# Optimization experiments

Hardware: AMD Instinct MI355X
Metric: run time of the kernel (lower is better)

Reference implementation:

```python
import jax, jax.numpy as jnp
import numpy as np

N_NODES = 100000
N_EDGES = 6400000
IN_CH = 128
NEG_SLOPE = 0.2


def setup_inputs() -> dict:
    key = jax.random.key(0)
    k1, k2, k3, k4, k5 = jax.random.split(key, 5)
    x = jax.random.normal(k1, (N_NODES, IN_CH), dtype=jnp.float32)
    edge_index = jax.random.randint(k2, (2, N_EDGES), 0, N_NODES, dtype=jnp.int64)
    # GATConv params (heads=1, out_channels=1): glorot-style scale
    W = jax.random.normal(k3, (IN_CH, 1), dtype=jnp.float32) / np.sqrt(IN_CH)
    att_src = jax.random.normal(k4, (1,), dtype=jnp.float32)
    att_dst = jax.random.normal(k5, (1,), dtype=jnp.float32)
    bias = jnp.zeros((1,), dtype=jnp.float32)
    return {"x": x, "edge_index": edge_index, "W": W,
            "att_src": att_src, "att_dst": att_dst, "bias": bias}


def reference(x, edge_index, W, att_src, att_dst, bias):
    N = x.shape[0]
    h = (x @ W)[:, 0]                      # [N] projected features (out_channels=1)
    # add self-loops (PyG default add_self_loops=True)
    loop = jnp.arange(N, dtype=edge_index.dtype)
    src = jnp.concatenate([edge_index[0], loop])   # [E+N]
    dst = jnp.concatenate([edge_index[1], loop])
    a_s = h * att_src[0]                   # per-node src attention term
    a_d = h * att_dst[0]                   # per-node dst attention term
    logits = jax.nn.leaky_relu(a_s[src] + a_d[dst], NEG_SLOPE)  # [E+N]
    # segment softmax over incoming edges of each destination node
    seg_max = jax.ops.segment_max(logits, dst, num_segments=N)
    e = jnp.exp(logits - seg_max[dst])
    denom = jax.ops.segment_sum(e, dst, num_segments=N)
    alpha = e / (denom[dst] + 1e-16)
    # scatter-aggregate weighted source features
    out = jax.ops.segment_sum(alpha * h[src], dst, num_segments=N)  # [N]
    return out[:, None] + bias             # [N, 1]
```

## Files before the change

kernel.cpp:

```cpp
#include <hip/hip_runtime.h>

#define IN_CH 128
#define NEG_SLOPE 0.2f
#define BINSZ 8000
#define NBINS 13
#define NW 8192
#define MAX_SG 39
#define MAX_BPB 40
#define PLACE_BLOCKS (NW / 4)
#define HMAX_BLOCKS 120
#define F_NUM 2097152.0f
#define F_DEN 16777216.0f
#define INV_F_NUM 4.76837158203125e-7f
#define INV_F_DEN 5.9604644775390625e-8f

typedef int   vi4 __attribute__((ext_vector_type(4)));
typedef float vf4 __attribute__((ext_vector_type(4)));

__device__ __forceinline__ float lrelu(float v) { return v > 0.f ? v : NEG_SLOPE * v; }
__device__ __forceinline__ unsigned enc_max(float f) {
    unsigned u = __float_as_uint(f);
    return (u & 0x80000000u) ? ~u : (u | 0x80000000u);
}
__device__ __forceinline__ float dec_max(unsigned e) {
    return (e & 0x80000000u) ? __uint_as_float(e ^ 0x80000000u) : __uint_as_float(~e);
}
__device__ __forceinline__ unsigned bf16_rne(float f) {
    unsigned u = __float_as_uint(f);
    return (u + 0x7FFFu + ((u >> 16) & 1u)) >> 16;
}

__device__ __forceinline__ void do_proj(const float* __restrict__ x, const float* __restrict__ W,
                                        const float* __restrict__ att_dst,
                                        float* __restrict__ h, float* __restrict__ ad_h,
                                        int n, int wid, int nwaves) {
    int lane = threadIdx.x & 63;
    int half = lane >> 5;
    int hl   = lane & 31;

    vf4 w4 = reinterpret_cast<const vf4*>(W)[hl];
    const float ad = att_dst[0];

    int npair = n >> 1;
    for (int p0 = wid * 4; p0 < npair; p0 += nwaves * 4) {
        float s[4];
        #pragma unroll
        for (int k = 0; k < 4; ++k) {
            int p = p0 + k;
            s[k] = 0.f;
            if (p < npair) {
                int row = 2 * p + half;
                vf4 v = __builtin_nontemporal_load(
                    reinterpret_cast<const vf4*>(x + (size_t)row * IN_CH) + hl);
                s[k] = v.x * w4.x + v.y * w4.y + v.z * w4.z + v.w * w4.w;
            }
        }
        #pragma unroll
        for (int k = 0; k < 4; ++k) {
            #pragma unroll
            for (int off = 16; off > 0; off >>= 1) s[k] += __shfl_xor(s[k], off);
        }
        #pragma unroll
        for (int k = 0; k < 4; ++k) {
            int p = p0 + k;
            if (p < npair && hl == 0) {
                int row = 2 * p + half;
                h[row] = s[k];
                ad_h[row] = s[k] * ad;
            }
        }
    }
    if ((n & 1) && wid == 0) {
        int row = n - 1;
        vf4 v = reinterpret_cast<const vf4*>(x + (size_t)row * IN_CH)[hl];
        float s = v.x * w4.x + v.y * w4.y + v.z * w4.z + v.w * w4.w;
        #pragma unroll
        for (int off = 16; off > 0; off >>= 1) s += __shfl_xor(s, off);
        if (lane == 0) { h[row] = s; ad_h[row] = s * ad; }
    }
}

__global__ __launch_bounds__(256)
void proj_kernel(const float* __restrict__ x, const float* __restrict__ W,
                 const float* __restrict__ att_dst,
                 float* __restrict__ h, float* __restrict__ ad_h, int n) {
    int wid    = (blockIdx.x * blockDim.x + threadIdx.x) >> 6;
    int nwaves = (gridDim.x * blockDim.x) >> 6;
    do_proj(x, W, att_dst, h, ad_h, n, wid, nwaves);
}

__global__ __launch_bounds__(256)
void count_proj_kernel(const int* __restrict__ dst_idx, int* __restrict__ wc, int E,
                       const float* __restrict__ x, const float* __restrict__ W,
                       const float* __restrict__ att_dst,
                       float* __restrict__ h, float* __restrict__ ad_h, int n) {
    __shared__ int cnt[4][NBINS];
    int b = blockIdx.x;
    int role = b % 3;
    if (role == 2) {
        int qid = b / 3;
        int wid = qid * 4 + (threadIdx.x >> 6);
        do_proj(x, W, att_dst, h, ad_h, n, wid, 4096);
        return;
    }
    int pid  = (b / 3) * 2 + role;
    int lane = threadIdx.x & 63, wv = threadIdx.x >> 6;
    int g = pid * 4 + wv;
    if (lane < NBINS) cnt[wv][lane] = 0;

    long long E4 = E >> 2;
    long long e0 = 4 * (E4 * g / NW);
    long long e1 = (g == NW - 1) ? (long long)E : 4 * (E4 * (g + 1) / NW);
    for (long long i0 = e0; i0 < e1; i0 += 256) {
        long long i = i0 + 4 * lane;
        if (i < e1) {
            vi4 d4 = __builtin_nontemporal_load(reinterpret_cast<const vi4*>(dst_idx + i));
            atomicAdd(&cnt[wv][d4.x / BINSZ], 1);
            atomicAdd(&cnt[wv][d4.y / BINSZ], 1);
            atomicAdd(&cnt[wv][d4.z / BINSZ], 1);
            atomicAdd(&cnt[wv][d4.w / BINSZ], 1);
        }
    }
    if (lane < NBINS) wc[lane * NW + g] = cnt[wv][lane];
}

__global__ __launch_bounds__(256)
void scanA_kernel(const int* __restrict__ wc, int* __restrict__ bsum) {
    __shared__ int wt[4];
    int t = threadIdx.x, lane = t & 63, wv = t >> 6;
    vi4 c = *reinterpret_cast<const vi4*>(wc + blockIdx.x * 1024 + 4 * t);
    int s = c.x + c.y + c.z + c.w;
    #pragma unroll
    for (int off = 32; off > 0; off >>= 1) s += __shfl_xor(s, off);
    if (lane == 0) wt[wv] = s;
    __syncthreads();
    if (t == 0) bsum[blockIdx.x] = wt[0] + wt[1] + wt[2] + wt[3];
}

__global__ __launch_bounds__(128)
void scanB_kernel(const int* __restrict__ bsum, int* __restrict__ bbase,
                  int* __restrict__ rbase, int* __restrict__ hist,
                  unsigned* __restrict__ maxenc, int nchunk) {
    __shared__ int sb[129];
    __shared__ int wt[2];
    int t = threadIdx.x, lane = t & 63, wv = t >> 6;
    if (t < 2) maxenc[t] = 0u;
    int v = (t < nchunk) ? bsum[t] : 0;
    int inc = v;
    #pragma unroll
    for (int d2 = 1; d2 < 64; d2 <<= 1) { int u = __shfl_up(inc, d2); if (lane >= d2) inc += u; }
    if (lane == 63) wt[wv] = inc;
    __syncthreads();
    int excl = ((wv == 1) ? wt[0] : 0) + inc - v;
    sb[t] = excl;
    if (t == 127) sb[128] = excl + v;
    __syncthreads();
    if (t < nchunk) bbase[t] = sb[t];
    if (t < NBINS) {
        int rb = sb[t * (NW / 1024)];
        rbase[t] = rb;
        int nb = (t == NBINS - 1) ? sb[128] : sb[(t + 1) * (NW / 1024)];
        hist[t] = nb - rb;
    }
}

__global__ __launch_bounds__(256)
void scanC_kernel(const int* __restrict__ wc, const int* __restrict__ bbase,
                  int* __restrict__ wbase) {
    __shared__ int wt[4];
    int t = threadIdx.x, lane = t & 63, wv = t >> 6;
    int base = blockIdx.x * 1024 + 4 * t;
    vi4 c = *reinterpret_cast<const vi4*>(wc + base);
    int s0 = c.x, s1 = s0 + c.y, s2 = s1 + c.z, s3 = s2 + c.w;
    int tot = s3;
    int inc = tot;
    #pragma unroll
    for (int d2 = 1; d2 < 64; d2 <<= 1) { int u = __shfl_up(inc, d2); if (lane >= d2) inc += u; }
    if (lane == 63) wt[wv] = inc;
    __syncthreads();
    int wb = 0;
    for (int k = 0; k < wv; ++k) wb += wt[k];
    int excl = bbase[blockIdx.x] + wb + inc - tot;
    vi4 o; o.x = excl; o.y = excl + s0; o.z = excl + s1; o.w = excl + s2;
    *reinterpret_cast<vi4*>(wbase + base) = o;
}

__global__ __launch_bounds__(256)
void place_hmax_kernel(const int* __restrict__ src_idx, const int* __restrict__ dst_idx,
                       const float* __restrict__ h, const int* __restrict__ wbase,
                       unsigned* __restrict__ rec, int E,
                       const float* __restrict__ att_src, const float* __restrict__ att_dst,
                       unsigned* __restrict__ maxenc, int n) {
    int b = blockIdx.x;
    if (b >= PLACE_BLOCKS) {
        int bid = b - PLACE_BLOCKS;
        const float as = att_src[0];
        const float ad = att_dst[0];
        float m1 = -1e30f, m2 = -1e30f;
        for (int i = bid * 256 + threadIdx.x; i < n; i += HMAX_BLOCKS * 256) {
            float v = h[i];
            m1 = fmaxf(m1, v * as);
            m2 = fmaxf(m2, v * ad);
        }
        #pragma unroll
        for (int off = 32; off > 0; off >>= 1) {
            m1 = fmaxf(m1, __shfl_xor(m1, off));
            m2 = fmaxf(m2, __shfl_xor(m2, off));
        }
        __shared__ float bm[2][4];
        int wv = threadIdx.x >> 6;
        if ((threadIdx.x & 63) == 0) { bm[0][wv] = m1; bm[1][wv] = m2; }
        __syncthreads();
        if (threadIdx.x == 0) {
            float a = fmaxf(fmaxf(bm[0][0], bm[0][1]), fmaxf(bm[0][2], bm[0][3]));
            float bmax = fmaxf(fmaxf(bm[1][0], bm[1][1]), fmaxf(bm[1][2], bm[1][3]));
            atomicMax(maxenc,     enc_max(a));
            atomicMax(maxenc + 1, enc_max(bmax));
        }
        return;
    }

    __shared__ int ccur[4][NBINS];
    int lane = threadIdx.x & 63, wv = threadIdx.x >> 6;
    int g = b * 4 + wv;
    if (lane < NBINS) ccur[wv][lane] = wbase[lane * NW + g];
    __syncthreads();

    long long E4 = E >> 2;
    long long e0 = 4 * (E4 * g / NW);
    long long e1 = (g == NW - 1) ? (long long)E : 4 * (E4 * (g + 1) / NW);

    long long i = e0 + 4 * (long long)lane;
    bool have = (i < e1);
    vi4 d4 = {0,0,0,0}, s4 = {0,0,0,0};
    if (have) {
        d4 = __builtin_nontemporal_load(reinterpret_cast<const vi4*>(dst_idx + i));
        s4 = __builtin_nontemporal_load(reinterpret_cast<const vi4*>(src_idx + i));
    }
    while (have) {
        long long nx = i + 256;
        bool nhave = (nx < e1);
        vi4 d4n = {0,0,0,0}, s4n = {0,0,0,0};
        if (nhave) {
            d4n = __builtin_nontemporal_load(reinterpret_cast<const vi4*>(dst_idx + nx));
            s4n = __builtin_nontemporal_load(reinterpret_cast<const vi4*>(src_idx + nx));
        }
        float h0 = h[s4.x], h1 = h[s4.y], h2 = h[s4.z], h3 = h[s4.w];
        int b0 = d4.x / BINSZ, b1 = d4.y / BINSZ, b2 = d4.z / BINSZ, b3 = d4.w / BINSZ;
        int p0 = atomicAdd(&ccur[wv][b0], 1);
        int p1 = atomicAdd(&ccur[wv][b1], 1);
        int p2 = atomicAdd(&ccur[wv][b2], 1);
        int p3 = atomicAdd(&ccur[wv][b3], 1);
        rec[p0] = ((unsigned)(d4.x - b0 * BINSZ) << 16) | bf16_rne(h0);
        rec[p1] = ((unsigned)(d4.y - b1 * BINSZ) << 16) | bf16_rne(h1);
        rec[p2] = ((unsigned)(d4.z - b2 * BINSZ) << 16) | bf16_rne(h2);
        rec[p3] = ((unsigned)(d4.w - b3 * BINSZ) << 16) | bf16_rne(h3);
        i = nx; d4 = d4n; s4 = s4n; have = nhave;
    }
}

__global__ __launch_bounds__(1024)
void gather_kernel(const unsigned* __restrict__ rec,
                   const float* __restrict__ ad_h,
                   const float* __restrict__ att_src, const unsigned* __restrict__ maxenc,
                   const int* __restrict__ rbase, const int* __restrict__ hist,
                   unsigned long long* __restrict__ part, int SG) {
    __shared__ __align__(16) unsigned long long s_acc[BINSZ];

    int bin   = blockIdx.x / SG;
    int slice = blockIdx.x - bin * SG;
    long long r0 = rbase[bin];
    int cnt   = hist[bin];
    long long g0 = r0 + (long long)cnt * slice / SG;
    long long g1 = r0 + (long long)cnt * (slice + 1) / SG;

    {
        vi4 z = {0, 0, 0, 0};
        for (int k = threadIdx.x; k < BINSZ / 2; k += 1024)
            *reinterpret_cast<vi4*>(&s_acc[2 * k]) = z;
    }
    __syncthreads();

    const float as = att_src[0];
    const float L  = lrelu(dec_max(maxenc[0]) + dec_max(maxenc[1]));
    const float* adw = ad_h + bin * BINSZ;

    auto process1 = [&](unsigned q) {
        int ri = q >> 16;
        float h0 = __uint_as_float(q << 16);
        float e0 = __expf(lrelu(fmaf(h0, as, adw[ri])) - L);
        unsigned long long p0 = ((unsigned long long)(long long)__float2int_rn(e0 * h0 * F_NUM) << 32)
                              + __float2uint_rn(e0 * F_DEN);
        atomicAdd(&s_acc[ri], p0);
    };

    long long a0 = (g0 + 3) & ~3LL;
    long long a1 = g1 & ~3LL;
    long long headEnd, tail0;
    if (a0 <= a1) { headEnd = a0; tail0 = a1; }
    else          { headEnd = g1; tail0 = g1; a0 = 0; a1 = 0; }

    for (long long i = g0 + threadIdx.x; i < headEnd; i += 1024) process1(rec[i]);

    long long i = a0 + 4 * (long long)threadIdx.x;
    vi4 q = {0,0,0,0};
    bool have = (i < a1);
    if (have) q = __builtin_nontemporal_load(reinterpret_cast<const vi4*>(rec + i));
    while (have) {
        long long nx = i + 4096;
        bool nhave = (nx < a1);
        vi4 nq = {0,0,0,0};
        if (nhave) nq = __builtin_nontemporal_load(reinterpret_cast<const vi4*>(rec + nx));
        unsigned u0=(unsigned)q.x, u1=(unsigned)q.y, u2=(unsigned)q.z, u3=(unsigned)q.w;
        int r0i=u0>>16, r1i=u1>>16, r2i=u2>>16, r3i=u3>>16;
        float h0=__uint_as_float(u0<<16), h1=__uint_as_float(u1<<16);
        float h2=__uint_as_float(u2<<16), h3=__uint_as_float(u3<<16);
        float e0 = __expf(lrelu(fmaf(h0, as, adw[r0i])) - L);
        float e1 = __expf(lrelu(fmaf(h1, as, adw[r1i])) - L);
        float e2 = __expf(lrelu(fmaf(h2, as, adw[r2i])) - L);
        float e3 = __expf(lrelu(fmaf(h3, as, adw[r3i])) - L);
        unsigned long long p0 = ((unsigned long long)(long long)__float2int_rn(e0 * h0 * F_NUM) << 32) + __float2uint_rn(e0 * F_DEN);
        unsigned long long p1 = ((unsigned long long)(long long)__float2int_rn(e1 * h1 * F_NUM) << 32) + __float2uint_rn(e1 * F_DEN);
        unsigned long long p2 = ((unsigned long long)(long long)__float2int_rn(e2 * h2 * F_NUM) << 32) + __float2uint_rn(e2 * F_DEN);
        unsigned long long p3 = ((unsigned long long)(long long)__float2int_rn(e3 * h3 * F_NUM) << 32) + __float2uint_rn(e3 * F_DEN);
        atomicAdd(&s_acc[r0i], p0);
        atomicAdd(&s_acc[r1i], p1);
        atomicAdd(&s_acc[r2i], p2);
        atomicAdd(&s_acc[r3i], p3);
        i = nx; q = nq; have = nhave;
    }

    for (long long i2 = tail0 + threadIdx.x; i2 < g1; i2 += 1024) process1(rec[i2]);
    __syncthreads();

    unsigned long long* outp = part + (size_t)blockIdx.x * BINSZ;
    for (int k = threadIdx.x; k < BINSZ / 2; k += 1024) {
        vi4 v = *reinterpret_cast<const vi4*>(&s_acc[2 * k]);
        __builtin_nontemporal_store(v, reinterpret_cast<vi4*>(outp + 2 * k));
    }
}

__global__ void reduce_final(const unsigned long long* __restrict__ part,
                             const float* __restrict__ h,
                             const float* __restrict__ att_src, const float* __restrict__ att_dst,
                             const float* __restrict__ bias, const unsigned* __restrict__ maxenc,
                             float* __restrict__ out, int n, int SG) {
    int i = blockIdx.x * blockDim.x + threadIdx.x;
    if (i >= n) return;
    int bin = i / BINSZ;
    int off = i - bin * BINSZ;
    float num = 0.f, den = 0.f;
    const unsigned long long* p = part + (size_t)(bin * SG) * BINSZ;
    for (int s = 0; s < SG; ++s) {
        unsigned long long v = __builtin_nontemporal_load(p + off);
        num += (float)(int)(v >> 32);
        den += (float)(unsigned)(v & 0xffffffffULL);
        p += BINSZ;
    }
    num *= INV_F_NUM;
    den *= INV_F_DEN;
    const float L = lrelu(dec_max(maxenc[0]) + dec_max(maxenc[1]));
    float hv = h[i];
    float e  = __expf(lrelu(hv * (att_src[0] + att_dst[0])) - L);
    out[i] = (num + e * hv) / (den + e + 1e-30f) + bias[0];
}

__global__ __launch_bounds__(1024)
void binpass_kernel(const int* __restrict__ src_idx, const int* __restrict__ dst_idx,
                    const float* __restrict__ h,
                    const float* __restrict__ att_src, const float* __restrict__ att_dst,
                    float* __restrict__ part, int E, int n, int BPB) {
    __shared__ float s_num[BINSZ];
    __shared__ float s_den[BINSZ];

    int bin   = blockIdx.x / BPB;
    int slice = blockIdx.x - bin * BPB;
    int base  = bin * BINSZ;
    int blen  = min(BINSZ, n - base);

    for (int k = threadIdx.x; k < BINSZ; k += 1024) { s_num[k] = 0.f; s_den[k] = 0.f; }
    __syncthreads();

    const float as = att_src[0];
    const float ad = att_dst[0];

    long long e0 = (long long)E * slice / BPB;
    long long e1 = (long long)E * (slice + 1) / BPB;
    for (long long i = e0 + threadIdx.x; i < e1; i += 1024) {
        int d = dst_idx[i];
        unsigned r = (unsigned)(d - base);
        if (r < (unsigned)blen) {
            int s = src_idx[i];
            float hs = h[s];
            float v  = fmaf(hs, as, h[d] * ad);
            float e  = __expf(lrelu(v));
            atomicAdd(&s_num[r], e * hs);
            atomicAdd(&s_den[r], e);
        }
    }
    __syncthreads();

    float* outp = part + (size_t)blockIdx.x * (2 * BINSZ);
    for (int k = threadIdx.x; k < BINSZ; k += 1024) {
        outp[k]         = s_num[k];
        outp[BINSZ + k] = s_den[k];
    }
}

__global__ void fb_reduce_final(const float* __restrict__ part, const float* __restrict__ h,
                                const float* __restrict__ att_src, const float* __restrict__ att_dst,
                                const float* __restrict__ bias, float* __restrict__ out,
                                int n, int BPB) {
    int i = blockIdx.x * blockDim.x + threadIdx.x;
    if (i >= n) return;
    int bin = i / BINSZ;
    int off = i - bin * BINSZ;
    float num = 0.f, den = 0.f;
    const float* p = part + (size_t)(bin * BPB) * (2 * BINSZ);
    for (int s = 0; s < BPB; ++s) {
        num += p[off];
        den += p[BINSZ + off];
        p += 2 * BINSZ;
    }
    float hv = h[i];
    float e  = __expf(lrelu(hv * (att_src[0] + att_dst[0])));
    out[i] = (num + e * hv) / (den + e + 1e-16f) + bias[0];
}

__global__ void edge_kernel(const int* __restrict__ src_idx, const int* __restrict__ dst_idx,
                            const float* __restrict__ h,
                            const float* __restrict__ att_src, const float* __restrict__ att_dst,
                            float* __restrict__ nd, int E) {
    const float as = att_src[0];
    const float ad = att_dst[0];
    int i      = blockIdx.x * blockDim.x + threadIdx.x;
    int stride = gridDim.x * blockDim.x;
    for (; i < E; i += stride) {
        int s = src_idx[i];
        int d = dst_idx[i];
        float hs = h[s];
        float e  = __expf(lrelu(fmaf(hs, as, h[d] * ad)));
        unsafeAtomicAdd(&nd[2 * d],     e * hs);
        unsafeAtomicAdd(&nd[2 * d + 1], e);
    }
}

__global__ void final_kernel(const float* __restrict__ h, const float* __restrict__ nd,
                             const float* __restrict__ att_src, const float* __restrict__ att_dst,
                             const float* __restrict__ bias, float* __restrict__ out, int n) {
    int i = blockIdx.x * blockDim.x + threadIdx.x;
    if (i >= n) return;
    float hv = h[i];
    float e  = __expf(lrelu(hv * (att_src[0] + att_dst[0])));
    out[i] = (nd[2 * i] + e * hv) / (nd[2 * i + 1] + e + 1e-16f) + bias[0];
}

extern "C" void kernel_launch(void* const* d_in, const int* in_sizes, int n_in,
                              void* d_out, int out_size, void* d_ws, size_t ws_size,
                              hipStream_t stream) {
    const float* x       = (const float*)d_in[0];
    const int*   ei      = (const int*)d_in[1];
    const float* W       = (const float*)d_in[2];
    const float* att_src = (const float*)d_in[3];
    const float* att_dst = (const float*)d_in[4];
    const float* bias    = (const float*)d_in[5];
    float*       out     = (float*)d_out;

    const int n = out_size;
    const int E = in_sizes[1] / 2;

    const int NELEM  = NBINS * NW;
    const int NCHUNK = NELEM / 1024;

    size_t off = 0;
    auto alloc = [&](size_t bytes) { size_t p = off; off = (off + bytes + 255) & ~(size_t)255; return p; };
    size_t o_h    = alloc((size_t)n * sizeof(float));
    size_t o_adh  = alloc((size_t)n * sizeof(float));
    size_t o_wc   = alloc((size_t)NELEM * sizeof(int));
    size_t o_wb   = alloc((size_t)NELEM * sizeof(int));
    size_t o_bs   = alloc((size_t)NCHUNK * sizeof(int));
    size_t o_bb   = alloc((size_t)NCHUNK * sizeof(int));
    size_t o_meta = alloc(64 * sizeof(int));
    size_t o_rec  = alloc((size_t)E * sizeof(unsigned));
    size_t fixed  = off;

    float*    h      = (float*)((char*)d_ws + o_h);
    float*    ad_h   = (float*)((char*)d_ws + o_adh);
    int*      rbase  = (int*)((char*)d_ws + o_meta);
    int*      hist   = rbase + 16;
    unsigned* maxenc = (unsigned*)(rbase + 32);
    const size_t per = (size_t)BINSZ * sizeof(unsigned long long);

    int SG = 0;
    if (ws_size > fixed) SG = (int)((ws_size - fixed) / ((size_t)NBINS * per));
    if (SG > MAX_SG) SG = MAX_SG;

    bool ok_shape = (n <= NBINS * BINSZ) && ((E & 3) == 0) && (E >= 4 * NW) && ((n & 1) == 0);

    if (SG >= 8 && ok_shape) {
        int*                wc   = (int*)((char*)d_ws + o_wc);
        int*                wb   = (int*)((char*)d_ws + o_wb);
        int*                bsum = (int*)((char*)d_ws + o_bs);
        int*                bbase= (int*)((char*)d_ws + o_bb);
        unsigned*           rec  = (unsigned*)((char*)d_ws + o_rec);
        unsigned long long* part = (unsigned long long*)((char*)d_ws + fixed);

        count_proj_kernel<<<3072, 256, 0, stream>>>(ei + E, wc, E,
                                                    x, W, att_dst, h, ad_h, n);
        scanA_kernel<<<NCHUNK, 256, 0, stream>>>(wc, bsum);
        scanB_kernel<<<1, 128, 0, stream>>>(bsum, bbase, rbase, hist, maxenc, NCHUNK);
        scanC_kernel<<<NCHUNK, 256, 0, stream>>>(wc, bbase, wb);
        place_hmax_kernel<<<PLACE_BLOCKS + HMAX_BLOCKS, 256, 0, stream>>>(
            ei, ei + E, h, wb, rec, E, att_src, att_dst, maxenc, n);
        gather_kernel<<<NBINS * SG, 1024, 0, stream>>>(rec, ad_h, att_src, maxenc,
                                                       rbase, hist, part, SG);
        reduce_final<<<(n + 255) / 256, 256, 0, stream>>>(part, h, att_src, att_dst,
                                                          bias, maxenc, out, n, SG);
    } else {
        proj_kernel<<<1024, 256, 0, stream>>>(x, W, att_dst, h, ad_h, n);
        size_t hb = (((size_t)n * 2 * sizeof(float)) + 255) & ~(size_t)255;
        int BPB = 0;
        if (ws_size > hb) BPB = (int)((ws_size - hb) / ((size_t)NBINS * per));
        if (BPB > MAX_BPB) BPB = MAX_BPB;

        if (BPB >= 6 && n <= NBINS * BINSZ) {
            float* part = (float*)((char*)d_ws + hb);
            binpass_kernel<<<NBINS * BPB, 1024, 0, stream>>>(
                ei, ei + E, h, att_src, att_dst, part, E, n, BPB);
            fb_reduce_final<<<(n + 255) / 256, 256, 0, stream>>>(
                part, h, att_src, att_dst, bias, out, n, BPB);
        } else {
            float* nd = (float*)((char*)d_ws + hb);
            hipMemsetAsync(nd, 0, (size_t)n * 2 * sizeof(float), stream);
            edge_kernel<<<2048, 256, 0, stream>>>(ei, ei + E, h, att_src, att_dst, nd, E);
            final_kernel<<<(n + 255) / 256, 256, 0, stream>>>(h, nd, att_src, att_dst,
                                                              bias, out, n);
        }
    }
}
```

Baseline: 116.5 us.

## Split placement and gather into halves to overlap second placement with first gather

Edge placement is split into two launches covering the first and second half of the wave groups. The gather for records placed by the first half runs in the same launch as the second half of placement, and a final kernel gathers the second half. The aim is to overlap scatter-placement memory traffic with the shared-memory atomic gather, at the cost of one more launch, doubled partial buffers, a longer reduce loop, and 1024-thread place blocks. Each half uses half as many gather slices per bin.

```diff
diff --git a/kernel.cpp b/kernel.cpp
--- a/kernel.cpp
+++ b/kernel.cpp
@@ -5,10 +5,10 @@
 #define BINSZ 8000
 #define NBINS 13
 #define NW 8192
-#define MAX_SG 39
+#define MAX_SGH 39
 #define MAX_BPB 40
-#define PLACE_BLOCKS (NW / 4)
-#define HMAX_BLOCKS 120
+#define PB1024 256
+#define HMAXB 30
 #define F_NUM 2097152.0f
 #define F_DEN 16777216.0f
 #define INV_F_NUM 4.76837158203125e-7f
@@ -185,50 +185,18 @@
     *reinterpret_cast<vi4*>(wbase + base) = o;
 }
 
-__global__ __launch_bounds__(256)
-void place_hmax_kernel(const int* __restrict__ src_idx, const int* __restrict__ dst_idx,
-                       const float* __restrict__ h, const int* __restrict__ wbase,
-                       unsigned* __restrict__ rec, int E,
-                       const float* __restrict__ att_src, const float* __restrict__ att_dst,
-                       unsigned* __restrict__ maxenc, int n) {
-    int b = blockIdx.x;
-    if (b >= PLACE_BLOCKS) {
-        int bid = b - PLACE_BLOCKS;
-        const float as = att_src[0];
-        const float ad = att_dst[0];
-        float m1 = -1e30f, m2 = -1e30f;
-        for (int i = bid * 256 + threadIdx.x; i < n; i += HMAX_BLOCKS * 256) {
-            float v = h[i];
-            m1 = fmaxf(m1, v * as);
-            m2 = fmaxf(m2, v * ad);
-        }
-        #pragma unroll
-        for (int off = 32; off > 0; off >>= 1) {
-            m1 = fmaxf(m1, __shfl_xor(m1, off));
-            m2 = fmaxf(m2, __shfl_xor(m2, off));
-        }
-        __shared__ float bm[2][4];
-        int wv = threadIdx.x >> 6;
-        if ((threadIdx.x & 63) == 0) { bm[0][wv] = m1; bm[1][wv] = m2; }
-        __syncthreads();
-        if (threadIdx.x == 0) {
-            float a = fmaxf(fmaxf(bm[0][0], bm[0][1]), fmaxf(bm[0][2], bm[0][3]));
-            float bmax = fmaxf(fmaxf(bm[1][0], bm[1][1]), fmaxf(bm[1][2], bm[1][3]));
-            atomicMax(maxenc,     enc_max(a));
-            atomicMax(maxenc + 1, enc_max(bmax));
-        }
-        return;
-    }
-
-    __shared__ int ccur[4][NBINS];
-    int lane = threadIdx.x & 63, wv = threadIdx.x >> 6;
-    int g = b * 4 + wv;
-    if (lane < NBINS) ccur[wv][lane] = wbase[lane * NW + g];
-    __syncthreads();
+__device__ __forceinline__ void place_wave(const int* __restrict__ src_idx,
+                                           const int* __restrict__ dst_idx,
+                                           const float* __restrict__ h,
+                                           const int* __restrict__ wbase,
+                                           unsigned* __restrict__ rec, int E,
+                                           int g, int* ccur) {
+    int lane = threadIdx.x & 63;
+    if (lane < NBINS) ccur[lane] = wbase[lane * NW + g];
 
     long long E4 = E >> 2;
-    long long e0 = 4 * (E4 * g / NW);
-    long long e1 = (g == NW - 1) ? (long long)E : 4 * (E4 * (g + 1) / NW);
+    long long e0 = 4 * (E4 * (long long)g / NW);
+    long long e1 = (g == NW - 1) ? (long long)E : 4 * (E4 * (long long)(g + 1) / NW);
 
     long long i = e0 + 4 * (long long)lane;
     bool have = (i < e1);
@@ -247,10 +215,10 @@
         }
         float h0 = h[s4.x], h1 = h[s4.y], h2 = h[s4.z], h3 = h[s4.w];
         int b0 = d4.x / BINSZ, b1 = d4.y / BINSZ, b2 = d4.z / BINSZ, b3 = d4.w / BINSZ;
-        int p0 = atomicAdd(&ccur[wv][b0], 1);
-        int p1 = atomicAdd(&ccur[wv][b1], 1);
-        int p2 = atomicAdd(&ccur[wv][b2], 1);
-        int p3 = atomicAdd(&ccur[wv][b3], 1);
+        int p0 = atomicAdd(&ccur[b0], 1);
+        int p1 = atomicAdd(&ccur[b1], 1);
+        int p2 = atomicAdd(&ccur[b2], 1);
+        int p3 = atomicAdd(&ccur[b3], 1);
         rec[p0] = ((unsigned)(d4.x - b0 * BINSZ) << 16) | bf16_rne(h0);
         rec[p1] = ((unsigned)(d4.y - b1 * BINSZ) << 16) | bf16_rne(h1);
         rec[p2] = ((unsigned)(d4.z - b2 * BINSZ) << 16) | bf16_rne(h2);
@@ -259,31 +227,18 @@
     }
 }
 
-__global__ __launch_bounds__(1024)
-void gather_kernel(const unsigned* __restrict__ rec,
-                   const float* __restrict__ ad_h,
-                   const float* __restrict__ att_src, const unsigned* __restrict__ maxenc,
-                   const int* __restrict__ rbase, const int* __restrict__ hist,
-                   unsigned long long* __restrict__ part, int SG) {
-    __shared__ __align__(16) unsigned long long s_acc[BINSZ];
-
-    int bin   = blockIdx.x / SG;
-    int slice = blockIdx.x - bin * SG;
-    long long r0 = rbase[bin];
-    int cnt   = hist[bin];
-    long long g0 = r0 + (long long)cnt * slice / SG;
-    long long g1 = r0 + (long long)cnt * (slice + 1) / SG;
-
+__device__ __forceinline__ void gather_range(const unsigned* __restrict__ rec,
+                                             const float* __restrict__ adw,
+                                             float as, float L,
+                                             long long g0, long long g1,
+                                             unsigned long long* s_acc,
+                                             unsigned long long* __restrict__ outp) {
     {
         vi4 z = {0, 0, 0, 0};
         for (int k = threadIdx.x; k < BINSZ / 2; k += 1024)
             *reinterpret_cast<vi4*>(&s_acc[2 * k]) = z;
     }
     __syncthreads();
-
-    const float as = att_src[0];
-    const float L  = lrelu(dec_max(maxenc[0]) + dec_max(maxenc[1]));
-    const float* adw = ad_h + bin * BINSZ;
 
     auto process1 = [&](unsigned q) {
         int ri = q >> 16;
@@ -333,29 +288,120 @@
     for (long long i2 = tail0 + threadIdx.x; i2 < g1; i2 += 1024) process1(rec[i2]);
     __syncthreads();
 
-    unsigned long long* outp = part + (size_t)blockIdx.x * BINSZ;
     for (int k = threadIdx.x; k < BINSZ / 2; k += 1024) {
         vi4 v = *reinterpret_cast<const vi4*>(&s_acc[2 * k]);
         __builtin_nontemporal_store(v, reinterpret_cast<vi4*>(outp + 2 * k));
     }
+}
+
+__global__ __launch_bounds__(1024)
+void place1_hmax_kernel(const int* __restrict__ src_idx, const int* __restrict__ dst_idx,
+                        const float* __restrict__ h, const int* __restrict__ wbase,
+                        unsigned* __restrict__ rec, int E,
+                        const float* __restrict__ att_src, const float* __restrict__ att_dst,
+                        unsigned* __restrict__ maxenc, int n) {
+    __shared__ int ccur[16][NBINS];
+    int b = blockIdx.x;
+    if (b < PB1024) {
+        int wv = threadIdx.x >> 6;
+        place_wave(src_idx, dst_idx, h, wbase, rec, E, b * 16 + wv, ccur[wv]);
+        return;
+    }
+    int bid = b - PB1024;
+    const float as = att_src[0];
+    const float ad = att_dst[0];
+    float m1 = -1e30f, m2 = -1e30f;
+    for (int i = bid * 1024 + threadIdx.x; i < n; i += HMAXB * 1024) {
+        float v = h[i];
+        m1 = fmaxf(m1, v * as);
+        m2 = fmaxf(m2, v * ad);
+    }
+    #pragma unroll
+    for (int off = 32; off > 0; off >>= 1) {
+        m1 = fmaxf(m1, __shfl_xor(m1, off));
+        m2 = fmaxf(m2, __shfl_xor(m2, off));
+    }
+    __shared__ float bm[2][16];
+    int wv = threadIdx.x >> 6;
+    if ((threadIdx.x & 63) == 0) { bm[0][wv] = m1; bm[1][wv] = m2; }
+    __syncthreads();
+    if (threadIdx.x == 0) {
+        float a = bm[0][0], bb = bm[1][0];
+        for (int k = 1; k < 16; ++k) { a = fmaxf(a, bm[0][k]); bb = fmaxf(bb, bm[1][k]); }
+        atomicMax(maxenc,     enc_max(a));
+        atomicMax(maxenc + 1, enc_max(bb));
+    }
+}
+
+__global__ __launch_bounds__(1024)
+void place2_gather1_kernel(const int* __restrict__ src_idx, const int* __restrict__ dst_idx,
+                           const float* __restrict__ h, const int* __restrict__ wbase,
+                           unsigned* __restrict__ rec, int E,
+                           const float* __restrict__ ad_h, const float* __restrict__ att_src,
+                           const unsigned* __restrict__ maxenc,
+                           const int* __restrict__ rbase,
+                           unsigned long long* __restrict__ part, int SGh) {
+    __shared__ int ccur[16][NBINS];
+    __shared__ __align__(16) unsigned long long s_acc[BINSZ];
+    int b = blockIdx.x;
+    if (b < PB1024) {
+        int wv = threadIdx.x >> 6;
+        place_wave(src_idx, dst_idx, h, wbase, rec, E, NW / 2 + b * 16 + wv, ccur[wv]);
+        return;
+    }
+    int gb    = b - PB1024;
+    int bin   = gb / SGh;
+    int slice = gb - bin * SGh;
+    long long lo  = rbase[bin];
+    long long mid = wbase[bin * NW + NW / 2];
+    long long cnt = mid - lo;
+    long long g0 = lo + cnt * slice / SGh;
+    long long g1 = lo + cnt * (slice + 1) / SGh;
+    const float as = att_src[0];
+    const float L  = lrelu(dec_max(maxenc[0]) + dec_max(maxenc[1]));
+    gather_range(rec, ad_h + bin * BINSZ, as, L, g0, g1, s_acc,
+                 part + (size_t)gb * BINSZ);
+}
+
+__global__ __launch_bounds__(1024)
+void gather2_kernel(const unsigned* __restrict__ rec, const int* __restrict__ wbase,
+                    const float* __restrict__ ad_h, const float* __restrict__ att_src,
+                    const unsigned* __restrict__ maxenc,
+                    const int* __restrict__ rbase, const int* __restrict__ hist,
+                    unsigned long long* __restrict__ part, int SGh) {
+    __shared__ __align__(16) unsigned long long s_acc[BINSZ];
+    int gb    = blockIdx.x;
+    int bin   = gb / SGh;
+    int slice = gb - bin * SGh;
+    long long mid = wbase[bin * NW + NW / 2];
+    long long hi  = (long long)rbase[bin] + hist[bin];
+    long long cnt = hi - mid;
+    long long g0 = mid + cnt * slice / SGh;
+    long long g1 = mid + cnt * (slice + 1) / SGh;
+    const float as = att_src[0];
+    const float L  = lrelu(dec_max(maxenc[0]) + dec_max(maxenc[1]));
+    gather_range(rec, ad_h + bin * BINSZ, as, L, g0, g1, s_acc,
+                 part + (size_t)(NBINS * SGh + gb) * BINSZ);
 }
 
 __global__ void reduce_final(const unsigned long long* __restrict__ part,
                              const float* __restrict__ h,
                              const float* __restrict__ att_src, const float* __restrict__ att_dst,
                              const float* __restrict__ bias, const unsigned* __restrict__ maxenc,
-                             float* __restrict__ out, int n, int SG) {
+                             float* __restrict__ out, int n, int SGh) {
     int i = blockIdx.x * blockDim.x + threadIdx.x;
     if (i >= n) return;
     int bin = i / BINSZ;
     int off = i - bin * BINSZ;
     float num = 0.f, den = 0.f;
-    const unsigned long long* p = part + (size_t)(bin * SG) * BINSZ;
-    for (int s = 0; s < SG; ++s) {
-        unsigned long long v = __builtin_nontemporal_load(p + off);
-        num += (float)(int)(v >> 32);
-        den += (float)(unsigned)(v & 0xffffffffULL);
-        p += BINSZ;
+    const unsigned long long* p1 = part + (size_t)(bin * SGh) * BINSZ;
+    const unsigned long long* p2 = part + (size_t)(NBINS * SGh + bin * SGh) * BINSZ;
+    for (int s = 0; s < SGh; ++s) {
+        unsigned long long v1 = __builtin_nontemporal_load(p1 + off);
+        unsigned long long v2 = __builtin_nontemporal_load(p2 + off);
+        num += (float)(int)(v1 >> 32) + (float)(int)(v2 >> 32);
+        den += (float)(unsigned)(v1 & 0xffffffffULL) + (float)(unsigned)(v2 & 0xffffffffULL);
+        p1 += BINSZ; p2 += BINSZ;
     }
     num *= INV_F_NUM;
     den *= INV_F_DEN;
@@ -491,13 +537,13 @@
     unsigned* maxenc = (unsigned*)(rbase + 32);
     const size_t per = (size_t)BINSZ * sizeof(unsigned long long);
 
-    int SG = 0;
-    if (ws_size > fixed) SG = (int)((ws_size - fixed) / ((size_t)NBINS * per));
-    if (SG > MAX_SG) SG = MAX_SG;
+    int SGh = 0;
+    if (ws_size > fixed) SGh = (int)((ws_size - fixed) / ((size_t)2 * NBINS * per));
+    if (SGh > MAX_SGH) SGh = MAX_SGH;
 
     bool ok_shape = (n <= NBINS * BINSZ) && ((E & 3) == 0) && (E >= 4 * NW) && ((n & 1) == 0);
 
-    if (SG >= 8 && ok_shape) {
+    if (SGh >= 4 && ok_shape) {
         int*                wc   = (int*)((char*)d_ws + o_wc);
         int*                wb   = (int*)((char*)d_ws + o_wb);
         int*                bsum = (int*)((char*)d_ws + o_bs);
@@ -510,12 +556,14 @@
         scanA_kernel<<<NCHUNK, 256, 0, stream>>>(wc, bsum);
         scanB_kernel<<<1, 128, 0, stream>>>(bsum, bbase, rbase, hist, maxenc, NCHUNK);
         scanC_kernel<<<NCHUNK, 256, 0, stream>>>(wc, bbase, wb);
-        place_hmax_kernel<<<PLACE_BLOCKS + HMAX_BLOCKS, 256, 0, stream>>>(
+        place1_hmax_kernel<<<PB1024 + HMAXB, 1024, 0, stream>>>(
             ei, ei + E, h, wb, rec, E, att_src, att_dst, maxenc, n);
-        gather_kernel<<<NBINS * SG, 1024, 0, stream>>>(rec, ad_h, att_src, maxenc,
-                                                       rbase, hist, part, SG);
+        place2_gather1_kernel<<<PB1024 + NBINS * SGh, 1024, 0, stream>>>(
+            ei, ei + E, h, wb, rec, E, ad_h, att_src, maxenc, rbase, part, SGh);
+        gather2_kernel<<<NBINS * SGh, 1024, 0, stream>>>(
+            rec, wb, ad_h, att_src, maxenc, rbase, hist, part, SGh);
         reduce_final<<<(n + 255) / 256, 256, 0, stream>>>(part, h, att_src, att_dst,
-                                                          bias, maxenc, out, n, SG);
+                                                          bias, maxenc, out, n, SGh);
     } else {
         proj_kernel<<<1024, 256, 0, stream>>>(x, W, att_dst, h, ad_h, n);
         size_t hb = (((size_t)n * 2 * sizeof(float)) + 255) & ~(size_t)255;
```

After: 125.1 us. 1.07x slower.
